# Kernel optimization log

Hardware: AMD Instinct MI355X
Metric: run time of the kernel (lower is better)

Reference implementation:

```python
import jax, jax.numpy as jnp
import numpy as np

SEQ, B, H, L = 1000, 256, 256, 10  # seq_len, batch, hidden(=input), num_layers


def setup_inputs() -> dict:
    key = jax.random.key(0)
    k0, k1, k2, k3, k4 = jax.random.split(key, 5)
    s = 1.0 / np.sqrt(H)  # torch LSTMCell init range
    return {
        "inputs": jax.random.normal(k0, (SEQ, B, H), jnp.float32),
        "W_ih": jax.random.uniform(k1, (L, 4 * H, H), jnp.float32, -s, s),
        "W_hh": jax.random.uniform(k2, (L, 4 * H, H), jnp.float32, -s, s),
        "b_ih": jax.random.uniform(k3, (L, 4 * H), jnp.float32, -s, s),
        "b_hh": jax.random.uniform(k4, (L, 4 * H), jnp.float32, -s, s),
    }


def _lstm_forward(inputs, W_ih, W_hh, b_ih, b_hh):
    # Faithful to the torch code, INCLUDING its h/c swap:
    #   torch:  c, h = cell(cur, (c, h))  with cell(in, (hx, cx)) -> (h', c')
    #   so hx := state_c, cx := state_h; state_c := h', state_h := c'; cur := state_h
    bsz = inputs.shape[1]
    sc0 = jnp.zeros((L, bsz, H), inputs.dtype)  # state_c list
    sh0 = jnp.zeros((L, bsz, H), inputs.dtype)  # state_h list

    def step(carry, x_t):
        sc, sh = carry
        cur = x_t
        sc_new, sh_new = [], []
        for j in range(L):  # fixed small layer stack
            gates = cur @ W_ih[j].T + b_ih[j] + sc[j] @ W_hh[j].T + b_hh[j]
            ii, ff, gg, oo = jnp.split(gates, 4, axis=-1)
            ii = jax.nn.sigmoid(ii)
            ff = jax.nn.sigmoid(ff)
            gg = jnp.tanh(gg)
            oo = jax.nn.sigmoid(oo)
            c_ret = ff * sh[j] + ii * gg        # LSTMCell's returned c'
            h_ret = oo * jnp.tanh(c_ret)        # LSTMCell's returned h'
            sc_new.append(h_ret)                # state_c[j] = h'
            sh_new.append(c_ret)                # state_h[j] = c'
            cur = c_ret                         # cur_input = state_h[j]
        return (jnp.stack(sc_new), jnp.stack(sh_new)), None

    (sc, sh), _ = jax.lax.scan(step, (sc0, sh0), inputs)
    return sh[L - 1]


def reference(inputs, W_ih, W_hh, b_ih, b_hh):
    return _lstm_forward(inputs, W_ih, W_hh, b_ih, b_hh)
```

## Files before the change

### kernel.cpp

```cpp
#include <hip/hip_runtime.h>

#define SEQ    1000
#define BATCH  256
#define HID    256
#define NL     10
#define G4H    1024
#define WELT   (NL * G4H * HID)
#define BH     (BATCH * HID)
#define NBLK   160
#define DSTR   32

typedef __bf16 bf16x8 __attribute__((ext_vector_type(8)));
typedef float  f32x4  __attribute__((ext_vector_type(4)));


__global__ __launch_bounds__(256) void lstm_prep(
    const float* __restrict__ Wih, const float* __restrict__ Whh,
    const float* __restrict__ bih, const float* __restrict__ bhh,
    __bf16* __restrict__ wih_bf, __bf16* __restrict__ whh_bf,
    float* __restrict__ biasc, __bf16* __restrict__ scb,
    unsigned int* __restrict__ done)
{
    const int i0 = blockIdx.x * blockDim.x + threadIdx.x;
    const int stride = gridDim.x * blockDim.x;
    for (int i = i0; i < WELT; i += stride) {
        wih_bf[i] = (__bf16)Wih[i];
        whh_bf[i] = (__bf16)Whh[i];
    }
    for (int i = i0; i < NL * G4H; i += stride) biasc[i] = bih[i] + bhh[i];
    for (int i = i0; i < NL * 2 * BH; i += stride) scb[i] = (__bf16)0.0f;
    if (i0 < NL * 4 * DSTR) done[i0] = 0u;
}

__device__ __forceinline__ void spin_ge(const unsigned int* p, unsigned int tgt)
{
    while (__hip_atomic_load(p, __ATOMIC_RELAXED, __HIP_MEMORY_SCOPE_AGENT) < tgt)
        __builtin_amdgcn_s_sleep(4);
}

__device__ __forceinline__ void ldg_coh(bf16x8& d, const __bf16* p)
{
    asm volatile("global_load_dwordx4 %0, %1, off sc0 sc1" : "=v"(d) : "v"(p));
}
__device__ __forceinline__ void ldg_l2(bf16x8& d, const __bf16* p)
{
    asm volatile("global_load_dwordx4 %0, %1, off sc0" : "=v"(d) : "v"(p));
}
__device__ __forceinline__ void stg_coh_b16(__bf16* p, __bf16 v)
{
    asm volatile("global_store_short %0, %1, off sc0 sc1" :: "v"(p), "v"(v) : "memory");
}
__device__ __forceinline__ void wait_vm0()
{
    asm volatile("s_waitcnt vmcnt(0)" ::: "memory");
}

__global__ __launch_bounds__(256, 1) void lstm_main(
    const float* __restrict__ x,
    const __bf16* __restrict__ wih_bf, const __bf16* __restrict__ whh_bf,
    const float* __restrict__ biasc,
    __bf16* __restrict__ scb, __bf16* __restrict__ cbuf,
    float* __restrict__ out, unsigned int* __restrict__ done)
{
    __shared__ __bf16 Alds[64][512];

    const int blk  = blockIdx.x;
    int j, tile;
    if (blk < 128) { j = blk & 7; tile = blk >> 3; }
    else           { j = 8 + ((blk & 7) >> 2); tile = ((blk & 3) << 2) | ((blk - 128) >> 3); }
    const int bt   = tile >> 2;
    const int b0   = bt << 6;
    const int h0   = (tile & 3) << 6;
    const int tid  = threadIdx.x;
    const int v    = tid >> 6;
    const int lane = tid & 63;
    const int m    = lane & 15;
    const int q    = lane >> 4;
    const int hw   = h0 + v * 16 + m;

    unsigned int* done_self = done + (j * 4 + bt) * DSTR;
    unsigned int* done_prod = done + ((j - 1) * 4 + bt) * DSTR;
    unsigned int* done_cons = done + ((j + 1) * 4 + bt) * DSTR;

    const __bf16* bihp[4];
    float biasg[4];
    bf16x8 wfhh[8][4];
#pragma unroll
    for (int g = 0; g < 4; ++g) {
        const size_t row = (size_t)j * G4H + g * HID + hw;
        bihp[g] = wih_bf + row * HID + q * 8;
        biasg[g] = biasc[(size_t)j * G4H + g * HID + hw];
        const __bf16* hh = whh_bf + row * HID + q * 8;
#pragma unroll
        for (int ch = 0; ch < 8; ++ch)
            wfhh[ch][g] = *(const bf16x8*)(hh + ch * 32);
    }

    float c_state[4][4];
#pragma unroll
    for (int bs = 0; bs < 4; ++bs)
#pragma unroll
        for (int r = 0; r < 4; ++r) c_state[bs][r] = 0.0f;

    for (int t = 0; t < SEQ; ++t) {
        const int par = t & 1;
        const __bf16* hprev = scb + (size_t)(j * 2 + ((t + 1) & 1)) * BH;
        __bf16* hout = scb + (size_t)(j * 2 + par) * BH;

        if (t >= 1) spin_ge(done_self, 4u * (unsigned)t);

        {
            bf16x8 tmp[8];
#pragma unroll
            for (int i = 0; i < 8; ++i) {
                const int row = i * 8 + v * 2 + (lane >> 5);
                const int c32 = lane & 31;
                ldg_l2(tmp[i], hprev + (size_t)(b0 + row) * HID + c32 * 8);
            }
            wait_vm0();
#pragma unroll
            for (int i = 0; i < 8; ++i) {
                const int row = i * 8 + v * 2 + (lane >> 5);
                const int c32 = lane & 31;
                const int cp  = (32 + c32) ^ (row & 7);
                *(bf16x8*)&Alds[0][(size_t)row * 512 + cp * 8] = tmp[i];
            }
        }
        __syncthreads();

        f32x4 acc[4][4];
#pragma unroll
        for (int g = 0; g < 4; ++g) {
            const float bb = biasg[g];
            const f32x4 bv = {bb, bb, bb, bb};
#pragma unroll
            for (int bs = 0; bs < 4; ++bs) acc[bs][g] = bv;
        }
#pragma unroll
        for (int ch = 0; ch < 8; ++ch) {
#pragma unroll
            for (int bs = 0; bs < 4; ++bs) {
                const int rowA = bs * 16 + m;
                const int cp = (32 + ch * 4 + q) ^ (rowA & 7);
                const bf16x8 af = *(const bf16x8*)&Alds[rowA][cp * 8];
#pragma unroll
                for (int g = 0; g < 4; ++g)
                    acc[bs][g] = __builtin_amdgcn_mfma_f32_16x16x32_bf16(
                        af, wfhh[ch][g], acc[bs][g], 0, 0, 0);
            }
        }

        if (j > 0) spin_ge(done_prod, 4u * (unsigned)(t + 1));
        if (j < NL - 1 && t >= 2) spin_ge(done_cons, 4u * (unsigned)(t - 1));

        if (j == 0) {
            const float* xt = x + (size_t)t * BH;
#pragma unroll
            for (int i = 0; i < 8; ++i) {
                const int row = i * 8 + v * 2 + (lane >> 5);
                const int c32 = lane & 31;
                const int cp  = c32 ^ (row & 7);
                const float4* p = (const float4*)(xt + (size_t)(b0 + row) * HID + c32 * 8);
                const float4 u0 = p[0];
                const float4 u1 = p[1];
                bf16x8 vv;
                vv[0] = (__bf16)u0.x; vv[1] = (__bf16)u0.y;
                vv[2] = (__bf16)u0.z; vv[3] = (__bf16)u0.w;
                vv[4] = (__bf16)u1.x; vv[5] = (__bf16)u1.y;
                vv[6] = (__bf16)u1.z; vv[7] = (__bf16)u1.w;
                *(bf16x8*)&Alds[0][(size_t)row * 512 + cp * 8] = vv;
            }
        } else {
            const __bf16* ct = cbuf + (size_t)((j - 1) * 2 + par) * BH;
            bf16x8 tmp[8];
#pragma unroll
            for (int i = 0; i < 8; ++i) {
                const int row = i * 8 + v * 2 + (lane >> 5);
                const int c32 = lane & 31;
                ldg_coh(tmp[i], ct + (size_t)(b0 + row) * HID + c32 * 8);
            }
            wait_vm0();
#pragma unroll
            for (int i = 0; i < 8; ++i) {
                const int row = i * 8 + v * 2 + (lane >> 5);
                const int c32 = lane & 31;
                const int cp  = c32 ^ (row & 7);
                *(bf16x8*)&Alds[0][(size_t)row * 512 + cp * 8] = tmp[i];
            }
        }
        __syncthreads();

#pragma unroll
        for (int ch = 0; ch < 8; ++ch) {
            bf16x8 bfr[4];
#pragma unroll
            for (int g = 0; g < 4; ++g)
                bfr[g] = *(const bf16x8*)(bihp[g] + ch * 32);
#pragma unroll
            for (int bs = 0; bs < 4; ++bs) {
                const int rowA = bs * 16 + m;
                const int cp = (ch * 4 + q) ^ (rowA & 7);
                const bf16x8 af = *(const bf16x8*)&Alds[rowA][cp * 8];
#pragma unroll
                for (int g = 0; g < 4; ++g)
                    acc[bs][g] = __builtin_amdgcn_mfma_f32_16x16x32_bf16(
                        af, bfr[g], acc[bs][g], 0, 0, 0);
            }
        }

        __bf16* cnext = (j < NL - 1) ? (cbuf + (size_t)(j * 2 + par) * BH) : (__bf16*)0;
#pragma unroll
        for (int bs = 0; bs < 4; ++bs) {
#pragma unroll
            for (int r = 0; r < 4; ++r) {
                const int b = b0 + bs * 16 + q * 4 + r;
                const float gi = acc[bs][0][r];
                const float gf = acc[bs][1][r];
                const float gg = acc[bs][2][r];
                const float go = acc[bs][3][r];
                const float ii = 1.0f / (1.0f + __expf(-gi));
                const float ff = 1.0f / (1.0f + __expf(-gf));
                const float tg = 1.0f - 2.0f / (__expf(2.0f * gg) + 1.0f);
                const float oo = 1.0f / (1.0f + __expf(-go));
                const float cn = ff * c_state[bs][r] + ii * tg;
                const float tc = 1.0f - 2.0f / (__expf(2.0f * cn) + 1.0f);
                const float hn = oo * tc;
                c_state[bs][r] = cn;
                hout[(size_t)b * HID + hw] = (__bf16)hn;
                if (j < NL - 1) {
                    stg_coh_b16(cnext + (size_t)b * HID + hw, (__bf16)cn);
                } else if (t == SEQ - 1) {
                    out[(size_t)b * HID + hw] = cn;
                }
            }
        }

        wait_vm0();
        __syncthreads();
        if (tid == 0)
            __hip_atomic_fetch_add(done_self, 1u, __ATOMIC_RELAXED,
                                   __HIP_MEMORY_SCOPE_AGENT);
    }
}

extern "C" void kernel_launch(void* const* d_in, const int* in_sizes, int n_in,
                              void* d_out, int out_size, void* d_ws, size_t ws_size,
                              hipStream_t stream)
{
    (void)in_sizes; (void)n_in; (void)out_size; (void)ws_size;
    const float* x   = (const float*)d_in[0];
    const float* Wih = (const float*)d_in[1];
    const float* Whh = (const float*)d_in[2];
    const float* bih = (const float*)d_in[3];
    const float* bhh = (const float*)d_in[4];
    float* out = (float*)d_out;

    char* ws = (char*)d_ws;
    __bf16* wih_bf = (__bf16*)(ws);
    __bf16* whh_bf = (__bf16*)(ws + 5242880);
    float*  biasc  = (float*) (ws + 10485760);
    __bf16* scb    = (__bf16*)(ws + 10526720);
    __bf16* cbuf   = (__bf16*)(ws + 13148160);
    unsigned int* done = (unsigned int*)(ws + 15507456);

    lstm_prep<<<dim3(1024), dim3(256), 0, stream>>>(
        Wih, Whh, bih, bhh, wih_bf, whh_bf, biasc, scb, done);
    lstm_main<<<dim3(NBLK), dim3(256), 0, stream>>>(
        x, wih_bf, whh_bf, biasc, scb, cbuf, out, done);
}
```

Baseline: 14.18 ms.

## Keep input-weight fragments in registers, move waits before barrier, use fast gate math

Each block now preloads its W_ih MFMA fragments into registers once, alongside W_hh, so the per-timestep global loads of input weights go away. The producer/consumer spin-waits move from after the recurrent MFMA to before the first barrier, done by a single lane in dedicated waves. Gate sigmoid/tanh switch to exp2 plus hardware reciprocal, and the spin sleep interval is shortened. Doubling the resident weight registers risks register pressure or spills. Moving the waits ahead of the barrier stops the recurrent MFMA from overlapping with the wait on the upstream layer.

```diff
diff --git a/kernel.cpp b/kernel.cpp
--- a/kernel.cpp
+++ b/kernel.cpp
@@ -35,9 +35,8 @@
 __device__ __forceinline__ void spin_ge(const unsigned int* p, unsigned int tgt)
 {
     while (__hip_atomic_load(p, __ATOMIC_RELAXED, __HIP_MEMORY_SCOPE_AGENT) < tgt)
-        __builtin_amdgcn_s_sleep(4);
-}
-
+        __builtin_amdgcn_s_sleep(2);
+}
 __device__ __forceinline__ void ldg_coh(bf16x8& d, const __bf16* p)
 {
     asm volatile("global_load_dwordx4 %0, %1, off sc0 sc1" : "=v"(d) : "v"(p));
@@ -53,6 +52,15 @@
 __device__ __forceinline__ void wait_vm0()
 {
     asm volatile("s_waitcnt vmcnt(0)" ::: "memory");
+}
+#define LOG2E 1.44269504f
+__device__ __forceinline__ float fsigmoid(float x)
+{
+    return __builtin_amdgcn_rcpf(1.0f + __builtin_amdgcn_exp2f(-x * LOG2E));
+}
+__device__ __forceinline__ float ftanh(float x)
+{
+    return 1.0f - 2.0f * __builtin_amdgcn_rcpf(1.0f + __builtin_amdgcn_exp2f(x * (2.0f * LOG2E)));
 }
 
 __global__ __launch_bounds__(256, 1) void lstm_main(
@@ -82,18 +90,20 @@
     unsigned int* done_prod = done + ((j - 1) * 4 + bt) * DSTR;
     unsigned int* done_cons = done + ((j + 1) * 4 + bt) * DSTR;
 
-    const __bf16* bihp[4];
     float biasg[4];
     bf16x8 wfhh[8][4];
+    bf16x8 wfih[8][4];
 #pragma unroll
     for (int g = 0; g < 4; ++g) {
         const size_t row = (size_t)j * G4H + g * HID + hw;
-        bihp[g] = wih_bf + row * HID + q * 8;
         biasg[g] = biasc[(size_t)j * G4H + g * HID + hw];
         const __bf16* hh = whh_bf + row * HID + q * 8;
-#pragma unroll
-        for (int ch = 0; ch < 8; ++ch)
+        const __bf16* ih = wih_bf + row * HID + q * 8;
+#pragma unroll
+        for (int ch = 0; ch < 8; ++ch) {
             wfhh[ch][g] = *(const bf16x8*)(hh + ch * 32);
+            wfih[ch][g] = *(const bf16x8*)(ih + ch * 32);
+        }
     }
 
     float c_state[4][4];
@@ -126,6 +136,9 @@
                 *(bf16x8*)&Alds[0][(size_t)row * 512 + cp * 8] = tmp[i];
             }
         }
+
+        if (v == 2 && j > 0 && lane == 0) spin_ge(done_prod, 4u * (unsigned)(t + 1));
+        if (v == 3 && j < NL - 1 && t >= 2 && lane == 0) spin_ge(done_cons, 4u * (unsigned)(t - 1));
         __syncthreads();
 
         f32x4 acc[4][4];
@@ -149,9 +162,6 @@
                         af, wfhh[ch][g], acc[bs][g], 0, 0, 0);
             }
         }
-
-        if (j > 0) spin_ge(done_prod, 4u * (unsigned)(t + 1));
-        if (j < NL - 1 && t >= 2) spin_ge(done_cons, 4u * (unsigned)(t - 1));
 
         if (j == 0) {
             const float* xt = x + (size_t)t * BH;
@@ -192,10 +202,6 @@
 
 #pragma unroll
         for (int ch = 0; ch < 8; ++ch) {
-            bf16x8 bfr[4];
-#pragma unroll
-            for (int g = 0; g < 4; ++g)
-                bfr[g] = *(const bf16x8*)(bihp[g] + ch * 32);
 #pragma unroll
             for (int bs = 0; bs < 4; ++bs) {
                 const int rowA = bs * 16 + m;
@@ -204,7 +210,7 @@
 #pragma unroll
                 for (int g = 0; g < 4; ++g)
                     acc[bs][g] = __builtin_amdgcn_mfma_f32_16x16x32_bf16(
-                        af, bfr[g], acc[bs][g], 0, 0, 0);
+                        af, wfih[ch][g], acc[bs][g], 0, 0, 0);
             }
         }
 
@@ -214,17 +220,12 @@
 #pragma unroll
             for (int r = 0; r < 4; ++r) {
                 const int b = b0 + bs * 16 + q * 4 + r;
-                const float gi = acc[bs][0][r];
-                const float gf = acc[bs][1][r];
-                const float gg = acc[bs][2][r];
-                const float go = acc[bs][3][r];
-                const float ii = 1.0f / (1.0f + __expf(-gi));
-                const float ff = 1.0f / (1.0f + __expf(-gf));
-                const float tg = 1.0f - 2.0f / (__expf(2.0f * gg) + 1.0f);
-                const float oo = 1.0f / (1.0f + __expf(-go));
+                const float ii = fsigmoid(acc[bs][0][r]);
+                const float ff = fsigmoid(acc[bs][1][r]);
+                const float tg = ftanh(acc[bs][2][r]);
+                const float oo = fsigmoid(acc[bs][3][r]);
                 const float cn = ff * c_state[bs][r] + ii * tg;
-                const float tc = 1.0f - 2.0f / (__expf(2.0f * cn) + 1.0f);
-                const float hn = oo * tc;
+                const float hn = oo * ftanh(cn);
                 c_state[bs][r] = cn;
                 hout[(size_t)b * HID + hw] = (__bf16)hn;
                 if (j < NL - 1) {
```

Measured after the change: 16.36 ms. 1.15x slower.
